# Optimization experiments

Measured on AMD Instinct MI355X. Metric: run time of the kernel, lower is better.

## Reference

```python
import jax, jax.numpy as jnp
import numpy as np


def _cdist(queries, data):
    # Euclidean distance matrix [m, n], matching torch.cdist(p=2)
    q2 = jnp.sum(queries * queries, axis=1)[:, None]
    d2 = jnp.sum(data * data, axis=1)[None, :]
    sq = q2 + d2 - 2.0 * (queries @ data.T)
    return jnp.sqrt(jnp.maximum(sq, 0.0))


def setup_inputs() -> dict:
    key = jax.random.key(0)
    k1, k2 = jax.random.split(key)
    data = jax.random.normal(k1, (16384, 3), dtype=jnp.float32)
    queries = jax.random.normal(k2, (16384, 3), dtype=jnp.float32)
    return {"data": data, "queries": queries, "n_neigbor": 32}


def reference(data, queries, n_neigbor):
    m = queries.shape[0]
    n = data.shape[0]
    dists = _cdist(queries, data)                      # [m, n]
    sorted_dist = jnp.sort(dists, axis=1)              # full row sort, as in original
    k = sorted_dist[:, n_neigbor]                      # (n_neigbor)-th smallest distance
    in_nbr = dists < k[:, None]                        # strictly-less -> exactly n_neigbor True per row (no ties)
    # nonzero() in the original emits column indices in ascending order per row.
    # Replicate with fixed shapes: map non-neighbors to sentinel n, sort, keep first n_neigbor.
    cols = jnp.where(in_nbr, jnp.arange(n, dtype=jnp.int64)[None, :], jnp.int64(n))
    neighbors_index = jnp.sort(cols, axis=1)[:, :n_neigbor].reshape(-1)  # [m * n_neigbor]
    counts = jnp.sum(in_nbr.astype(jnp.int64), axis=1)
    splits = jnp.concatenate([jnp.zeros((1,), dtype=jnp.int64), jnp.cumsum(counts)])  # [m+1]
    return neighbors_index, splits
```

## Files before the change

### kernel.cpp

```cpp
#include <hip/hip_runtime.h>
#include <stdint.h>

typedef unsigned long long u64;
typedef unsigned int u32;

#define NQ 16384
#define ND 16384
#define KNB 32
#define KK 33
#define SPLITS_BASE (NQ * KNB)
#define CAP 512
#define NRR (CAP / 64)
#define NWQ 4
#define G 36
#define G3 (G*G*G)
#define SCB ((G3 + 255) / 256)
#define FINF (__int_as_float(0x7f800000))


template<int BITS>
__device__ __forceinline__ int wave_sum_small(int v) {
    int tot = 0;
    #pragma unroll
    for (int b = 0; b < BITS; ++b)
        tot += (int)__popcll(__ballot((v >> b) & 1)) << b;
    return tot;
}
__device__ __forceinline__ float wave_max_f(float v) {
    #pragma unroll
    for (int s = 1; s < 64; s <<= 1) v = fmaxf(v, __shfl_xor(v, s, 64));
    return v;
}
__device__ __forceinline__ int wave_excl_prefix(int v, int lane) {
    int x = v;
    #pragma unroll
    for (int s = 1; s < 64; s <<= 1) {
        const int y = __shfl_up(x, s, 64);
        if (lane >= s) x += y;
    }
    return x - v;
}
__device__ __forceinline__ int iclamp(int v, int lo, int hi) {
    return v < lo ? lo : (v > hi ? hi : v);
}
__device__ __forceinline__ u32 fenc(float f) {
    const u32 u = __float_as_uint(f);
    return (u & 0x80000000u) ? ~u : (u | 0x80000000u);
}
__device__ __forceinline__ float fdec(u32 e) {
    const u32 u = (e & 0x80000000u) ? (e & 0x7fffffffu) : ~e;
    return __uint_as_float(u);
}

__device__ __forceinline__ float bisect_rank8(const float (&r)[NRR], int rank) {
    u32 lo = 0u, hi = 0x7f800000u;
    #pragma unroll 1
    while (lo < hi) {
        const u32 mid = (lo + hi) >> 1;
        const float pv = __uint_as_float(mid);
        int c = 0;
        #pragma unroll
        for (int j = 0; j < NRR; ++j) c += (r[j] <= pv) ? 1 : 0;
        const int tot = wave_sum_small<4>(c);
        if (tot >= rank) hi = mid; else lo = mid + 1;
    }
    return __uint_as_float(hi);
}

__device__ __forceinline__ void pool_prune(float* kp, u32* ip, int& cnt, float& Tk,
                                           int lane, u64 lt) {
    float m = FINF;
    #pragma unroll 1
    for (int j = lane; j < cnt; j += 64) m = fminf(m, kp[j]);
    const float M = wave_max_f(m);
    int nc = 0;
    #pragma unroll 1
    for (int j0 = 0; j0 < cnt; j0 += 64) {
        const int j = j0 + lane;
        const bool val = j < cnt;
        float k = FINF; u32 id = 0;
        if (val) { k = kp[j]; id = ip[j]; }
        const bool keep = val && (k <= M);
        const u64 mask = __ballot(keep);
        if (keep) {
            const int s = nc + (int)__popcll(mask & lt);
            kp[s] = k; ip[s] = id;
        }
        nc += (int)__popcll(mask);
    }
    cnt = nc; Tk = M;
}

__device__ __forceinline__ void pool_hard_prune(float* kp, u32* ip, int& cnt,
                                                int lane, u64 lt) {
    float r[NRR];
    #pragma unroll
    for (int j = 0; j < NRR; ++j) {
        const int s = j * 64 + lane;
        r[j] = (s < cnt) ? kp[s] : FINF;
    }
    const float v = bisect_rank8(r, 64);
    int nc = 0, eqs = 0;
    #pragma unroll 1
    for (int j0 = 0; j0 < cnt; j0 += 64) {
        const int j = j0 + lane;
        const bool val = j < cnt;
        float k = FINF; u32 id = 0;
        if (val) { k = kp[j]; id = ip[j]; }
        const bool lt_v = val && (k < v);
        const bool eq_v = val && (k == v);
        const u64 mlt = __ballot(lt_v);
        const u64 meq = __ballot(eq_v);
        const int poplt = (int)__popcll(mlt);
        const int popeq = (int)__popcll(meq);
        if (lt_v) { const int s = nc + (int)__popcll(mlt & lt); kp[s] = k; ip[s] = id; }
        if (eq_v) {
            const int pe = (int)__popcll(meq & lt);
            if (eqs + pe < 64) { const int s = nc + poplt + pe; kp[s] = k; ip[s] = id; }
        }
        int kept_eq = popeq;
        if (eqs + popeq > 64) kept_eq = (64 - eqs > 0) ? (64 - eqs) : 0;
        nc += poplt + kept_eq;
        eqs += popeq;
    }
    cnt = nc;
}

__global__ __launch_bounds__(256) void bbox_kernel(const float* __restrict__ data,
                                                   u32* __restrict__ bbe) {
    const int i = blockIdx.x * 256 + threadIdx.x;
    const int lane = threadIdx.x & 63;
    float x = data[3*i], y = data[3*i+1], z = data[3*i+2];
    float mnx = x, mny = y, mnz = z, mxx = x, mxy = y, mxz = z;
    #pragma unroll
    for (int s = 1; s < 64; s <<= 1) {
        mnx = fminf(mnx, __shfl_xor(mnx, s, 64)); mxx = fmaxf(mxx, __shfl_xor(mxx, s, 64));
        mny = fminf(mny, __shfl_xor(mny, s, 64)); mxy = fmaxf(mxy, __shfl_xor(mxy, s, 64));
        mnz = fminf(mnz, __shfl_xor(mnz, s, 64)); mxz = fmaxf(mxz, __shfl_xor(mxz, s, 64));
    }
    if (lane == 0) {
        atomicMin(&bbe[0], fenc(mnx)); atomicMin(&bbe[1], fenc(mny)); atomicMin(&bbe[2], fenc(mnz));
        atomicMax(&bbe[3], fenc(mxx)); atomicMax(&bbe[4], fenc(mxy)); atomicMax(&bbe[5], fenc(mxz));
    }
}

__device__ __forceinline__ void grid_geom(const u32* bbe, float& mnx, float& mny, float& mnz,
                                          float& hx, float& hy, float& hz) {
    mnx = fdec(bbe[0]); mny = fdec(bbe[1]); mnz = fdec(bbe[2]);
    hx = fmaxf((fdec(bbe[3]) - mnx) * (1.0f / G), 1e-20f);
    hy = fmaxf((fdec(bbe[4]) - mny) * (1.0f / G), 1e-20f);
    hz = fmaxf((fdec(bbe[5]) - mnz) * (1.0f / G), 1e-20f);
}

__device__ __forceinline__ u32 cell_of(const u32* bbe, float x, float y, float z) {
    float mnx, mny, mnz, hx, hy, hz;
    grid_geom(bbe, mnx, mny, mnz, hx, hy, hz);
    const int cx = iclamp((int)((x - mnx) / hx), 0, G-1);
    const int cy = iclamp((int)((y - mny) / hy), 0, G-1);
    const int cz = iclamp((int)((z - mnz) / hz), 0, G-1);
    return (u32)((cz * G + cy) * G + cx);
}

__global__ __launch_bounds__(256) void cellid_hist(const float* __restrict__ data,
                                                   const u32* __restrict__ bbe,
                                                   u32* __restrict__ hist) {
    const int i = blockIdx.x * 256 + threadIdx.x;
    atomicAdd(&hist[cell_of(bbe, data[3*i], data[3*i+1], data[3*i+2])], 1u);
}

__global__ __launch_bounds__(256) void scan_partial(const u32* __restrict__ hist,
                                                    u32* __restrict__ cstart,
                                                    u32* __restrict__ bsum) {
    __shared__ u32 lds[256];
    const int t = threadIdx.x;
    const int i = blockIdx.x * 256 + t;
    const u32 v = (i < G3) ? hist[i] : 0u;
    lds[t] = v;
    __syncthreads();
    u32 x = v;
    for (int off = 1; off < 256; off *= 2) {
        const u32 add = (t >= off) ? lds[t - off] : 0u;
        __syncthreads();
        x += add; lds[t] = x;
        __syncthreads();
    }
    if (i < G3) cstart[i] = x - v;
    if (t == 255) bsum[blockIdx.x] = x;
}

__global__ __launch_bounds__(256) void scan_bsums(u32* __restrict__ bsum) {
    __shared__ u32 lds[256];
    const int t = threadIdx.x;
    const u32 v = (t < SCB) ? bsum[t] : 0u;
    lds[t] = v;
    __syncthreads();
    u32 x = v;
    for (int off = 1; off < 256; off *= 2) {
        const u32 add = (t >= off) ? lds[t - off] : 0u;
        __syncthreads();
        x += add; lds[t] = x;
        __syncthreads();
    }
    if (t < SCB) bsum[t] = x - v;
}

__global__ __launch_bounds__(256) void scan_add(u32* __restrict__ cstart,
                                                u32* __restrict__ cursor,
                                                const u32* __restrict__ bsum) {
    const int i = blockIdx.x * 256 + threadIdx.x;
    if (i < G3) {
        const u32 val = cstart[i] + bsum[blockIdx.x];
        cstart[i] = val; cursor[i] = val;
    }
    if (i == 0) cstart[G3] = (u32)ND;
}

__global__ __launch_bounds__(256) void scatter(const float* __restrict__ data,
                                               const u32* __restrict__ bbe,
                                               u32* __restrict__ cursor,
                                               float4* __restrict__ pts) {
    const int i = blockIdx.x * 256 + threadIdx.x;
    const float x = data[3*i], y = data[3*i+1], z = data[3*i+2];
    const u32 pos = atomicAdd(&cursor[cell_of(bbe, x, y, z)], 1u);
    pts[pos] = make_float4(x, y, z, __uint_as_float((u32)i));
}

__global__ __launch_bounds__(256) void knn_grid(const float4* __restrict__ pts,
                                                const u32* __restrict__ cstart,
                                                const float* __restrict__ queries,
                                                const u32* __restrict__ bbe,
                                                int* __restrict__ out_nb,
                                                int* __restrict__ splits) {
    __shared__ float keyP[NWQ][CAP];
    __shared__ u32   idxP[NWQ][CAP];
    __shared__ int   accI[NWQ][KNB];

    const int lane = threadIdx.x & 63;
    const int wid  = threadIdx.x >> 6;
    const int q = blockIdx.x * NWQ + wid;
    const u64 lt = (1ull << lane) - 1ull;
    float* kp = keyP[wid];
    u32*   ip = idxP[wid];

    const float qx = queries[3*q], qy = queries[3*q+1], qz = queries[3*q+2];
    const float q2 = __fadd_rn(__fadd_rn(__fmul_rn(qx,qx), __fmul_rn(qy,qy)), __fmul_rn(qz,qz));

    float mnx, mny, mnz, hx, hy, hz;
    grid_geom(bbe, mnx, mny, mnz, hx, hy, hz);
    const float hmin = fminf(hx, fminf(hy, hz));
    const int cx = iclamp((int)((qx - mnx) / hx), 0, G-1);
    const int cy = iclamp((int)((qy - mny) / hy), 0, G-1);
    const int cz = iclamp((int)((qz - mnz) / hz), 0, G-1);

    float Tk = FINF;
    int cnt = 0;

    auto gather_batch = [&](int sA, int lA, int sB, int lB) {
        const int len = lA + lB;
        const int P = wave_excl_prefix(len, lane);
        const int T = __shfl(P + len, 63, 64);
        #pragma unroll 1
        for (int g0 = 0; g0 < T; g0 += 64) {
            const int pos = g0 + lane;
            const bool val = pos < T;
            int rsel = 0;
            #pragma unroll
            for (int st = 32; st >= 1; st >>= 1) {
                const int t = rsel + st;
                const int Pt = __shfl(P, t, 64);
                if (Pt <= pos) rsel = t;
            }
            const int Pr  = __shfl(P,  rsel, 64);
            const int sAr = __shfl(sA, rsel, 64);
            const int lAr = __shfl(lA, rsel, 64);
            const int sBr = __shfl(sB, rsel, 64);
            const int off = pos - Pr;
            const int pi = (off < lAr) ? (sAr + off) : (sBr + (off - lAr));
            float key = FINF; u32 oi = 0; bool acc = false;
            if (val) {
                const float4 w = pts[pi];
                oi = __float_as_uint(w.w);
                const float d2 = __fadd_rn(__fadd_rn(__fmul_rn(w.x,w.x), __fmul_rn(w.y,w.y)),
                                           __fmul_rn(w.z,w.z));
                const float dot = __fmaf_rn(qz, w.z, __fmaf_rn(qy, w.y, __fmul_rn(qx, w.x)));
                const float sq  = __fsub_rn(__fadd_rn(q2, d2), __fadd_rn(dot, dot));
                key = fmaxf(sq, 0.0f);
                acc = key <= Tk;
            }
            const u64 mask = __ballot(acc);
            if (mask) {
                if (acc) {
                    const int s = cnt + (int)__popcll(mask & lt);
                    kp[s] = key; ip[s] = oi;
                }
                cnt += (int)__popcll(mask);
                if (cnt > CAP - 64) {
                    pool_prune(kp, ip, cnt, Tk, lane, lt);
                    if (cnt > CAP - 64) pool_hard_prune(kp, ip, cnt, lane, lt);
                }
            }
        }
    };

    int W = 0;
    {
        int ccount = 0;
        while (ccount < KK && W < G) {
            ++W;
            const int side = 2*W + 1, nrows = side * side;
            ccount = 0;
            for (int r0 = 0; r0 < nrows; r0 += 64) {
                const int rid = r0 + lane;
                int len = 0;
                if (rid < nrows) {
                    const int dz = rid / side - W, dy = rid % side - W;
                    const int zz = cz + dz, yy = cy + dy;
                    if (zz >= 0 && zz < G && yy >= 0 && yy < G) {
                        const int xlo = cx - W < 0 ? 0 : cx - W;
                        const int xhi = cx + W > G-1 ? G-1 : cx + W;
                        const int rb = (zz * G + yy) * G;
                        len = (int)cstart[rb + xhi + 1] - (int)cstart[rb + xlo];
                    }
                }
                ccount += wave_sum_small<6>(len < 63 ? len : 63);
            }
        }
    }

    {
        const int side = 2*W + 1, nrows = side * side;
        for (int r0 = 0; r0 < nrows; r0 += 64) {
            const int rid = r0 + lane;
            int sA = 0, lA = 0;
            if (rid < nrows) {
                const int dz = rid / side - W, dy = rid % side - W;
                const int zz = cz + dz, yy = cy + dy;
                if (zz >= 0 && zz < G && yy >= 0 && yy < G) {
                    const int xlo = cx - W < 0 ? 0 : cx - W;
                    const int xhi = cx + W > G-1 ? G-1 : cx + W;
                    const int rb = (zz * G + yy) * G;
                    sA = (int)cstart[rb + xlo];
                    lA = (int)cstart[rb + xhi + 1] - sA;
                }
            }
            gather_batch(sA, lA, 0, 0);
        }
    }

    float k33b;
    if (cnt <= 64) {
        float v = (lane < cnt) ? kp[lane] : FINF;
        #pragma unroll
        for (int k = 2; k <= 64; k <<= 1) {
            #pragma unroll
            for (int j = k >> 1; j >= 1; j >>= 1) {
                const float o = __shfl_xor(v, j, 64);
                const bool up = ((lane & k) == 0);
                const bool keepmin = (((lane & j) == 0) == up);
                v = keepmin ? fminf(v, o) : fmaxf(v, o);
            }
        }
        k33b = __shfl(v, KK - 1, 64);
    } else {
        float r[NRR];
        #pragma unroll
        for (int j = 0; j < NRR; ++j) {
            const int s = j * 64 + lane;
            r[j] = (s < cnt) ? kp[s] : FINF;
        }
        k33b = bisect_rank8(r, KK);
    }

    {
        int nc = 0;
        #pragma unroll 1
        for (int j0 = 0; j0 < cnt; j0 += 64) {
            const int j = j0 + lane;
            const bool val = j < cnt;
            float k = FINF; u32 id = 0;
            if (val) { k = kp[j]; id = ip[j]; }
            const bool keep = val && (k <= k33b);
            const u64 mask = __ballot(keep);
            if (keep) {
                const int s = nc + (int)__popcll(mask & lt);
                kp[s] = k; ip[s] = id;
            }
            nc += (int)__popcll(mask);
        }
        cnt = nc; Tk = k33b;
    }

    const float R2m = __fmaf_rn(k33b, 1.0002f, 1e-3f);
    if (!(R2m < (float)W * (float)W * hmin * hmin)) {
        const float Rm = sqrtf(R2m);
        const int Dz = (int)fminf(floorf(Rm / hz) + 1.0f, (float)G);
        const int Dy = (int)fminf(floorf(Rm / hy) + 1.0f, (float)G);
        const int sidey = 2*Dy + 1;
        const int nrows = (2*Dz + 1) * sidey;
        for (int r0 = 0; r0 < nrows; r0 += 64) {
            const int rid = r0 + lane;
            int sA = 0, lA = 0, sB = 0, lB = 0;
            if (rid < nrows) {
                const int dz = rid / sidey - Dz;
                const int dy = rid % sidey - Dy;
                const int zz = cz + dz, yy = cy + dy;
                if (zz >= 0 && zz < G && yy >= 0 && yy < G) {
                    const int adz = dz < 0 ? -dz : dz;
                    const int ady = dy < 0 ? -dy : dy;
                    const float mz = (adz >= 1) ? (float)(adz - 1) * hz : 0.0f;
                    const float my = (ady >= 1) ? (float)(ady - 1) * hy : 0.0f;
                    const float rowmin2 = mz*mz + my*my;
                    if (rowmin2 <= R2m) {
                        const int dxr = (int)fminf(floorf(sqrtf(R2m - rowmin2) / hx) + 1.0f, (float)G);
                        const int xlo = cx - dxr < 0 ? 0 : cx - dxr;
                        const int xhi = cx + dxr > G-1 ? G-1 : cx + dxr;
                        if (xlo <= xhi) {
                            const int rb = (zz * G + yy) * G;
                            if (adz <= W && ady <= W) {
                                const int xhiA = (cx - W - 1 < xhi) ? cx - W - 1 : xhi;
                                const int xloB = (cx + W + 1 > xlo) ? cx + W + 1 : xlo;
                                if (xlo <= xhiA) {
                                    sA = (int)cstart[rb + xlo];
                                    lA = (int)cstart[rb + xhiA + 1] - sA;
                                }
                                if (xloB <= xhi) {
                                    sB = (int)cstart[rb + xloB];
                                    lB = (int)cstart[rb + xhi + 1] - sB;
                                }
                            } else {
                                sA = (int)cstart[rb + xlo];
                                lA = (int)cstart[rb + xhi + 1] - sA;
                            }
                        }
                    }
                }
            }
            gather_batch(sA, lA, sB, lB);
        }
    }

    float k33;
    if (cnt <= 64) {
        float v = (lane < cnt) ? kp[lane] : FINF;
        #pragma unroll
        for (int k = 2; k <= 64; k <<= 1) {
            #pragma unroll
            for (int j = k >> 1; j >= 1; j >>= 1) {
                const float o = __shfl_xor(v, j, 64);
                const bool up = ((lane & k) == 0);
                const bool keepmin = (((lane & j) == 0) == up);
                v = keepmin ? fminf(v, o) : fmaxf(v, o);
            }
        }
        k33 = __shfl(v, KK - 1, 64);
    } else {
        float r[NRR];
        #pragma unroll
        for (int j = 0; j < NRR; ++j) {
            const int s = j * 64 + lane;
            r[j] = (s < cnt) ? kp[s] : FINF;
        }
        k33 = bisect_rank8(r, KK);
    }

    const float kd = sqrtf(k33);
    float cut;
    if (!(kd > 0.0f)) {
        cut = -1.0f;
    } else {
        int bi = __float_as_int(__fmul_rn(kd, kd));
        #pragma unroll 1
        for (int s = 0; s < 8; ++s) {
            if (bi > 0 && sqrtf(__int_as_float(bi - 1)) >= kd) --bi; else break;
        }
        #pragma unroll 1
        for (int s = 0; s < 8; ++s) {
            if (sqrtf(__int_as_float(bi)) < kd) ++bi; else break;
        }
        cut = __int_as_float(bi);
    }

    int c = 0;
    #pragma unroll 1
    for (int j0 = 0; j0 < cnt; j0 += 64) {
        const int j = j0 + lane;
        const bool val = j < cnt;
        const float k = val ? kp[j] : FINF;
        const bool keep = val && (k < cut);
        const u64 mask = __ballot(keep);
        if (keep) {
            const int s = c + (int)__popcll(mask & lt);
            if (s < KNB) accI[wid][s] = (int)ip[j];
        }
        c += (int)__popcll(mask);
    }
    if (c > KNB) c = KNB;

    if (lane < KNB) {
        if (lane < c) {
            const int my = accI[wid][lane];
            int rank = 0;
            #pragma unroll 1
            for (int j = 0; j < KNB; ++j)
                if (j < c) rank += (accI[wid][j] < my) ? 1 : 0;
            out_nb[(size_t)q * KNB + rank] = my;
        } else {
            out_nb[(size_t)q * KNB + lane] = ND;
        }
    }
    if (lane == 0) splits[1 + q] = c;
}

__global__ __launch_bounds__(256) void knn_direct_kernel(const float* __restrict__ data,
                                                         const float* __restrict__ queries,
                                                         int* __restrict__ out_nb,
                                                         int* __restrict__ splits) {
    __shared__ float4 tile[1024];
    const int q = blockIdx.x * 256 + threadIdx.x;
    const float qx = queries[3*q], qy = queries[3*q+1], qz = queries[3*q+2];
    const float q2 = __fadd_rn(__fadd_rn(__fmul_rn(qx,qx), __fmul_rn(qy,qy)), __fmul_rn(qz,qz));
    float arrk[KK]; int arri[KK];
    for (int j = 0; j < KK; ++j) { arrk[j] = FINF; arri[j] = ND; }
    float cur_maxk = FINF;
    for (int t0 = 0; t0 < ND; t0 += 1024) {
        for (int p = threadIdx.x; p < 1024; p += 256) {
            const int g = t0 + p;
            const float x = data[3*g], y = data[3*g+1], z = data[3*g+2];
            const float d2 = __fadd_rn(__fadd_rn(__fmul_rn(x,x), __fmul_rn(y,y)), __fmul_rn(z,z));
            tile[p] = make_float4(x, y, z, d2);
        }
        __syncthreads();
        for (int p = 0; p < 1024; ++p) {
            const float4 dp = tile[p];
            const float dot = __fmaf_rn(qz, dp.z, __fmaf_rn(qy, dp.y, __fmul_rn(qx, dp.x)));
            const float sq  = __fsub_rn(__fadd_rn(q2, dp.w), __fadd_rn(dot, dot));
            const float key = fmaxf(sq, 0.0f);
            if (key < cur_maxk) {
                int mp = 0; float m = -1.0f;
                for (int j = 0; j < KK; ++j) if (arrk[j] > m) { m = arrk[j]; mp = j; }
                arrk[mp] = key; arri[mp] = t0 + p;
                m = -1.0f;
                for (int j = 0; j < KK; ++j) if (arrk[j] > m) m = arrk[j];
                cur_maxk = m;
            }
        }
        __syncthreads();
    }
    const float kdist = sqrtf(cur_maxk);
    int acc[KNB]; int c = 0;
    for (int j = 0; j < KK; ++j) {
        const float d = sqrtf(arrk[j]);
        if (d < kdist && c < KNB) acc[c++] = arri[j];
    }
    for (int a = 1; a < c; ++a) {
        const int v = acc[a]; int j = a;
        while (j > 0 && acc[j-1] > v) { acc[j] = acc[j-1]; --j; }
        acc[j] = v;
    }
    int* row = out_nb + (size_t)q * KNB;
    for (int j = 0; j < KNB; ++j) row[j] = (j < c) ? acc[j] : ND;
    splits[1 + q] = c;
}

__global__ __launch_bounds__(1024) void splits_scan_kernel(int* __restrict__ splits) {
    __shared__ int lds[1024];
    const int t = threadIdx.x;
    int v[16]; int s = 0;
    #pragma unroll
    for (int j = 0; j < 16; ++j) { v[j] = splits[1 + t*16 + j]; s += v[j]; }
    lds[t] = s;
    __syncthreads();
    for (int off = 1; off < 1024; off *= 2) {
        const int add = (t >= off) ? lds[t - off] : 0;
        __syncthreads();
        lds[t] += add;
        __syncthreads();
    }
    int run = lds[t] - s;
    #pragma unroll
    for (int j = 0; j < 16; ++j) { run += v[j]; splits[1 + t*16 + j] = run; }
    if (t == 0) splits[0] = 0;
}

extern "C" void kernel_launch(void* const* d_in, const int* in_sizes, int n_in,
                              void* d_out, int out_size, void* d_ws, size_t ws_size,
                              hipStream_t stream) {
    const float* data    = (const float*)d_in[0];
    const float* queries = (const float*)d_in[1];
    int* out    = (int*)d_out;
    int* splits = out + SPLITS_BASE;

    const size_t bb_off     = 0;
    const size_t hist_off   = 64;
    const size_t cstart_off = hist_off + (size_t)G3 * 4;
    const size_t cursor_off = cstart_off + (size_t)(G3 + 1) * 4;
    const size_t bsum_off   = cursor_off + (size_t)G3 * 4;
    size_t pts_off          = bsum_off + 256 * 4;
    pts_off = (pts_off + 255) & ~(size_t)255;
    const size_t need       = pts_off + (size_t)ND * 16;

    if (ws_size >= need) {
        u32*    bbe    = (u32*)((char*)d_ws + bb_off);
        u32*    hist   = (u32*)((char*)d_ws + hist_off);
        u32*    cstart = (u32*)((char*)d_ws + cstart_off);
        u32*    cursor = (u32*)((char*)d_ws + cursor_off);
        u32*    bsum   = (u32*)((char*)d_ws + bsum_off);
        float4* pts    = (float4*)((char*)d_ws + pts_off);

        hipMemsetAsync(bbe, 0xFF, 12, stream);
        hipMemsetAsync((char*)bbe + 12, 0x00, 12, stream);
        hipMemsetAsync(hist, 0x00, (size_t)G3 * 4, stream);
        hipLaunchKernelGGL(bbox_kernel, dim3(ND / 256), dim3(256), 0, stream, data, bbe);
        hipLaunchKernelGGL(cellid_hist, dim3(ND / 256), dim3(256), 0, stream, data, bbe, hist);
        hipLaunchKernelGGL(scan_partial, dim3(SCB), dim3(256), 0, stream, hist, cstart, bsum);
        hipLaunchKernelGGL(scan_bsums, dim3(1), dim3(256), 0, stream, bsum);
        hipLaunchKernelGGL(scan_add, dim3(SCB), dim3(256), 0, stream, cstart, cursor, bsum);
        hipLaunchKernelGGL(scatter, dim3(ND / 256), dim3(256), 0, stream, data, bbe, cursor, pts);
        hipLaunchKernelGGL(knn_grid, dim3(NQ / NWQ), dim3(256), 0, stream,
                           pts, cstart, queries, bbe, out, splits);
    } else {
        hipLaunchKernelGGL(knn_direct_kernel, dim3(NQ / 256), dim3(256), 0, stream,
                           data, queries, out, splits);
    }
    hipLaunchKernelGGL(splits_scan_kernel, dim3(1), dim3(1024), 0, stream, splits);
}
```

Measured before the change: 117.4 us.

## Fuse grid build into one cooperative kernel and halve waves per KNN block

Replaces the three memsets and six small build kernels (bbox, histogram, three scan stages, scatter) with one cooperative kernel that uses grid-wide syncs between phases. The aim is to remove the launch and inter-kernel gaps that dominate such tiny kernels. Separately, the KNN kernel now runs 2 waves per block instead of 4, giving smaller blocks and finer scheduling. Grid syncs carry their own cost, and cooperative launch needs all 256 blocks to be resident at once.

```diff
diff --git a/kernel.cpp b/kernel.cpp
--- a/kernel.cpp
+++ b/kernel.cpp
@@ -1,4 +1,5 @@
 #include <hip/hip_runtime.h>
+#include <hip/hip_cooperative_groups.h>
 #include <stdint.h>
 
 typedef unsigned long long u64;
@@ -11,10 +12,9 @@
 #define SPLITS_BASE (NQ * KNB)
 #define CAP 512
 #define NRR (CAP / 64)
-#define NWQ 4
+#define NWQ 2
 #define G 36
 #define G3 (G*G*G)
-#define SCB ((G3 + 255) / 256)
 #define FINF (__int_as_float(0x7f800000))
 
 
@@ -126,24 +126,6 @@
     cnt = nc;
 }
 
-__global__ __launch_bounds__(256) void bbox_kernel(const float* __restrict__ data,
-                                                   u32* __restrict__ bbe) {
-    const int i = blockIdx.x * 256 + threadIdx.x;
-    const int lane = threadIdx.x & 63;
-    float x = data[3*i], y = data[3*i+1], z = data[3*i+2];
-    float mnx = x, mny = y, mnz = z, mxx = x, mxy = y, mxz = z;
-    #pragma unroll
-    for (int s = 1; s < 64; s <<= 1) {
-        mnx = fminf(mnx, __shfl_xor(mnx, s, 64)); mxx = fmaxf(mxx, __shfl_xor(mxx, s, 64));
-        mny = fminf(mny, __shfl_xor(mny, s, 64)); mxy = fmaxf(mxy, __shfl_xor(mxy, s, 64));
-        mnz = fminf(mnz, __shfl_xor(mnz, s, 64)); mxz = fmaxf(mxz, __shfl_xor(mxz, s, 64));
-    }
-    if (lane == 0) {
-        atomicMin(&bbe[0], fenc(mnx)); atomicMin(&bbe[1], fenc(mny)); atomicMin(&bbe[2], fenc(mnz));
-        atomicMax(&bbe[3], fenc(mxx)); atomicMax(&bbe[4], fenc(mxy)); atomicMax(&bbe[5], fenc(mxz));
-    }
-}
-
 __device__ __forceinline__ void grid_geom(const u32* bbe, float& mnx, float& mny, float& mnz,
                                           float& hx, float& hy, float& hz) {
     mnx = fdec(bbe[0]); mny = fdec(bbe[1]); mnz = fdec(bbe[2]);
@@ -161,76 +143,95 @@
     return (u32)((cz * G + cy) * G + cx);
 }
 
-__global__ __launch_bounds__(256) void cellid_hist(const float* __restrict__ data,
-                                                   const u32* __restrict__ bbe,
-                                                   u32* __restrict__ hist) {
-    const int i = blockIdx.x * 256 + threadIdx.x;
-    atomicAdd(&hist[cell_of(bbe, data[3*i], data[3*i+1], data[3*i+2])], 1u);
-}
-
-__global__ __launch_bounds__(256) void scan_partial(const u32* __restrict__ hist,
-                                                    u32* __restrict__ cstart,
-                                                    u32* __restrict__ bsum) {
+__global__ __launch_bounds__(256) void build_all(const float* __restrict__ data,
+                                                 u32* __restrict__ bbe,
+                                                 u32* __restrict__ hist,
+                                                 u32* __restrict__ cstart,
+                                                 u32* __restrict__ cursor,
+                                                 u32* __restrict__ bsum,
+                                                 float4* __restrict__ pts) {
+    cooperative_groups::grid_group gg = cooperative_groups::this_grid();
     __shared__ u32 lds[256];
-    const int t = threadIdx.x;
-    const int i = blockIdx.x * 256 + t;
-    const u32 v = (i < G3) ? hist[i] : 0u;
-    lds[t] = v;
+    const int tid = threadIdx.x;
+    const int bid = blockIdx.x;
+    const int gt = bid * 256 + tid;
+    const int lane = tid & 63;
+
+    for (int i = gt; i < G3; i += 65536) hist[i] = 0u;
+    if (gt < 3) bbe[gt] = 0xFFFFFFFFu;
+    else if (gt < 6) bbe[gt] = 0u;
+    gg.sync();
+
+    if (gt < ND) {
+        float x = data[3*gt], y = data[3*gt+1], z = data[3*gt+2];
+        float mnx = x, mny = y, mnz = z, mxx = x, mxy = y, mxz = z;
+        #pragma unroll
+        for (int s = 1; s < 64; s <<= 1) {
+            mnx = fminf(mnx, __shfl_xor(mnx, s, 64)); mxx = fmaxf(mxx, __shfl_xor(mxx, s, 64));
+            mny = fminf(mny, __shfl_xor(mny, s, 64)); mxy = fmaxf(mxy, __shfl_xor(mxy, s, 64));
+            mnz = fminf(mnz, __shfl_xor(mnz, s, 64)); mxz = fmaxf(mxz, __shfl_xor(mxz, s, 64));
+        }
+        if (lane == 0) {
+            atomicMin(&bbe[0], fenc(mnx)); atomicMin(&bbe[1], fenc(mny)); atomicMin(&bbe[2], fenc(mnz));
+            atomicMax(&bbe[3], fenc(mxx)); atomicMax(&bbe[4], fenc(mxy)); atomicMax(&bbe[5], fenc(mxz));
+        }
+    }
+    gg.sync();
+
+    if (gt < ND)
+        atomicAdd(&hist[cell_of(bbe, data[3*gt], data[3*gt+1], data[3*gt+2])], 1u);
+    gg.sync();
+
+    const u32 hv = (gt < G3) ? hist[gt] : 0u;
+    lds[tid] = hv;
     __syncthreads();
-    u32 x = v;
+    u32 x = hv;
     for (int off = 1; off < 256; off *= 2) {
-        const u32 add = (t >= off) ? lds[t - off] : 0u;
-        __syncthreads();
-        x += add; lds[t] = x;
-        __syncthreads();
-    }
-    if (i < G3) cstart[i] = x - v;
-    if (t == 255) bsum[blockIdx.x] = x;
-}
-
-__global__ __launch_bounds__(256) void scan_bsums(u32* __restrict__ bsum) {
-    __shared__ u32 lds[256];
-    const int t = threadIdx.x;
-    const u32 v = (t < SCB) ? bsum[t] : 0u;
-    lds[t] = v;
-    __syncthreads();
-    u32 x = v;
-    for (int off = 1; off < 256; off *= 2) {
-        const u32 add = (t >= off) ? lds[t - off] : 0u;
-        __syncthreads();
-        x += add; lds[t] = x;
-        __syncthreads();
-    }
-    if (t < SCB) bsum[t] = x - v;
-}
-
-__global__ __launch_bounds__(256) void scan_add(u32* __restrict__ cstart,
-                                                u32* __restrict__ cursor,
-                                                const u32* __restrict__ bsum) {
-    const int i = blockIdx.x * 256 + threadIdx.x;
-    if (i < G3) {
-        const u32 val = cstart[i] + bsum[blockIdx.x];
-        cstart[i] = val; cursor[i] = val;
-    }
-    if (i == 0) cstart[G3] = (u32)ND;
-}
-
-__global__ __launch_bounds__(256) void scatter(const float* __restrict__ data,
-                                               const u32* __restrict__ bbe,
-                                               u32* __restrict__ cursor,
-                                               float4* __restrict__ pts) {
-    const int i = blockIdx.x * 256 + threadIdx.x;
-    const float x = data[3*i], y = data[3*i+1], z = data[3*i+2];
-    const u32 pos = atomicAdd(&cursor[cell_of(bbe, x, y, z)], 1u);
-    pts[pos] = make_float4(x, y, z, __uint_as_float((u32)i));
-}
-
-__global__ __launch_bounds__(256) void knn_grid(const float4* __restrict__ pts,
-                                                const u32* __restrict__ cstart,
-                                                const float* __restrict__ queries,
-                                                const u32* __restrict__ bbe,
-                                                int* __restrict__ out_nb,
-                                                int* __restrict__ splits) {
+        const u32 add = (tid >= off) ? lds[tid - off] : 0u;
+        __syncthreads();
+        x += add; lds[tid] = x;
+        __syncthreads();
+    }
+    if (gt < G3) cstart[gt] = x - hv;
+    if (tid == 255) bsum[bid] = x;
+    gg.sync();
+
+    {
+        const u32 bv = bsum[tid];
+        __syncthreads();
+        lds[tid] = bv;
+        __syncthreads();
+        u32 y = bv;
+        for (int off = 1; off < 256; off *= 2) {
+            const u32 add = (tid >= off) ? lds[tid - off] : 0u;
+            __syncthreads();
+            y += add; lds[tid] = y;
+            __syncthreads();
+        }
+        const u32 boff = lds[bid] - ((bid == tid) ? bv : 0u) - ((bid == tid) ? 0u : 0u);
+        const u32 excl = lds[bid] - bsum[bid];
+        if (gt < G3) {
+            const u32 val = (x - hv) + excl;
+            cstart[gt] = val; cursor[gt] = val;
+        }
+        if (gt == 0) cstart[G3] = (u32)ND;
+        (void)boff;
+    }
+    gg.sync();
+
+    if (gt < ND) {
+        const float px = data[3*gt], py = data[3*gt+1], pz = data[3*gt+2];
+        const u32 pos = atomicAdd(&cursor[cell_of(bbe, px, py, pz)], 1u);
+        pts[pos] = make_float4(px, py, pz, __uint_as_float((u32)gt));
+    }
+}
+
+__global__ __launch_bounds__(64 * NWQ) void knn_grid(const float4* __restrict__ pts,
+                                                     const u32* __restrict__ cstart,
+                                                     const float* __restrict__ queries,
+                                                     const u32* __restrict__ bbe,
+                                                     int* __restrict__ out_nb,
+                                                     int* __restrict__ splits) {
     __shared__ float keyP[NWQ][CAP];
     __shared__ u32   idxP[NWQ][CAP];
     __shared__ int   accI[NWQ][KNB];
@@ -607,16 +608,11 @@
         u32*    bsum   = (u32*)((char*)d_ws + bsum_off);
         float4* pts    = (float4*)((char*)d_ws + pts_off);
 
-        hipMemsetAsync(bbe, 0xFF, 12, stream);
-        hipMemsetAsync((char*)bbe + 12, 0x00, 12, stream);
-        hipMemsetAsync(hist, 0x00, (size_t)G3 * 4, stream);
-        hipLaunchKernelGGL(bbox_kernel, dim3(ND / 256), dim3(256), 0, stream, data, bbe);
-        hipLaunchKernelGGL(cellid_hist, dim3(ND / 256), dim3(256), 0, stream, data, bbe, hist);
-        hipLaunchKernelGGL(scan_partial, dim3(SCB), dim3(256), 0, stream, hist, cstart, bsum);
-        hipLaunchKernelGGL(scan_bsums, dim3(1), dim3(256), 0, stream, bsum);
-        hipLaunchKernelGGL(scan_add, dim3(SCB), dim3(256), 0, stream, cstart, cursor, bsum);
-        hipLaunchKernelGGL(scatter, dim3(ND / 256), dim3(256), 0, stream, data, bbe, cursor, pts);
-        hipLaunchKernelGGL(knn_grid, dim3(NQ / NWQ), dim3(256), 0, stream,
+        void* args[] = { (void*)&data, (void*)&bbe, (void*)&hist, (void*)&cstart,
+                         (void*)&cursor, (void*)&bsum, (void*)&pts };
+        hipLaunchCooperativeKernel((const void*)build_all, dim3(256), dim3(256),
+                                   args, 0, stream);
+        hipLaunchKernelGGL(knn_grid, dim3(NQ / NWQ), dim3(64 * NWQ), 0, stream,
                            pts, cstart, queries, bbe, out, splits);
     } else {
         hipLaunchKernelGGL(knn_direct_kernel, dim3(NQ / 256), dim3(256), 0, stream,
```

New measurement: 220.1 us. +87.4%, slower.

## Fold memsets and block-sum scan into neighbouring kernels, halve knn block size

Applied to the files above, without the earlier changes.

Encodes the bounding-box max as a negated min so a single 0xFF memset initialises all six entries. The histogram zeroing moves into bbox_kernel, and the block-sum scan is recomputed redundantly inside each scan_add block, which removes two memsets and one kernel launch. knn_grid now runs two query waves per block instead of four, giving smaller blocks and less LDS per block. The trade is redundant scan work in every scan_add block in return for fewer launches on a short pipeline.

```diff
diff --git a/kernel.cpp b/kernel.cpp
--- a/kernel.cpp
+++ b/kernel.cpp
@@ -11,7 +11,7 @@
 #define SPLITS_BASE (NQ * KNB)
 #define CAP 512
 #define NRR (CAP / 64)
-#define NWQ 4
+#define NWQ 2
 #define G 36
 #define G3 (G*G*G)
 #define SCB ((G3 + 255) / 256)
@@ -126,30 +126,13 @@
     cnt = nc;
 }
 
-__global__ __launch_bounds__(256) void bbox_kernel(const float* __restrict__ data,
-                                                   u32* __restrict__ bbe) {
-    const int i = blockIdx.x * 256 + threadIdx.x;
-    const int lane = threadIdx.x & 63;
-    float x = data[3*i], y = data[3*i+1], z = data[3*i+2];
-    float mnx = x, mny = y, mnz = z, mxx = x, mxy = y, mxz = z;
-    #pragma unroll
-    for (int s = 1; s < 64; s <<= 1) {
-        mnx = fminf(mnx, __shfl_xor(mnx, s, 64)); mxx = fmaxf(mxx, __shfl_xor(mxx, s, 64));
-        mny = fminf(mny, __shfl_xor(mny, s, 64)); mxy = fmaxf(mxy, __shfl_xor(mxy, s, 64));
-        mnz = fminf(mnz, __shfl_xor(mnz, s, 64)); mxz = fmaxf(mxz, __shfl_xor(mxz, s, 64));
-    }
-    if (lane == 0) {
-        atomicMin(&bbe[0], fenc(mnx)); atomicMin(&bbe[1], fenc(mny)); atomicMin(&bbe[2], fenc(mnz));
-        atomicMax(&bbe[3], fenc(mxx)); atomicMax(&bbe[4], fenc(mxy)); atomicMax(&bbe[5], fenc(mxz));
-    }
-}
-
 __device__ __forceinline__ void grid_geom(const u32* bbe, float& mnx, float& mny, float& mnz,
                                           float& hx, float& hy, float& hz) {
     mnx = fdec(bbe[0]); mny = fdec(bbe[1]); mnz = fdec(bbe[2]);
-    hx = fmaxf((fdec(bbe[3]) - mnx) * (1.0f / G), 1e-20f);
-    hy = fmaxf((fdec(bbe[4]) - mny) * (1.0f / G), 1e-20f);
-    hz = fmaxf((fdec(bbe[5]) - mnz) * (1.0f / G), 1e-20f);
+    const float mxx = -fdec(bbe[3]), mxy = -fdec(bbe[4]), mxz = -fdec(bbe[5]);
+    hx = fmaxf((mxx - mnx) * (1.0f / G), 1e-20f);
+    hy = fmaxf((mxy - mny) * (1.0f / G), 1e-20f);
+    hz = fmaxf((mxz - mnz) * (1.0f / G), 1e-20f);
 }
 
 __device__ __forceinline__ u32 cell_of(const u32* bbe, float x, float y, float z) {
@@ -159,6 +142,26 @@
     const int cy = iclamp((int)((y - mny) / hy), 0, G-1);
     const int cz = iclamp((int)((z - mnz) / hz), 0, G-1);
     return (u32)((cz * G + cy) * G + cx);
+}
+
+__global__ __launch_bounds__(256) void bbox_kernel(const float* __restrict__ data,
+                                                   u32* __restrict__ bbe,
+                                                   u32* __restrict__ hist) {
+    const int i = blockIdx.x * 256 + threadIdx.x;
+    for (int h = i; h < G3; h += ND) hist[h] = 0u;
+    const int lane = threadIdx.x & 63;
+    const float x = data[3*i], y = data[3*i+1], z = data[3*i+2];
+    float mnx = x, mny = y, mnz = z, nx = -x, ny = -y, nz = -z;
+    #pragma unroll
+    for (int s = 1; s < 64; s <<= 1) {
+        mnx = fminf(mnx, __shfl_xor(mnx, s, 64)); nx = fminf(nx, __shfl_xor(nx, s, 64));
+        mny = fminf(mny, __shfl_xor(mny, s, 64)); ny = fminf(ny, __shfl_xor(ny, s, 64));
+        mnz = fminf(mnz, __shfl_xor(mnz, s, 64)); nz = fminf(nz, __shfl_xor(nz, s, 64));
+    }
+    if (lane == 0) {
+        atomicMin(&bbe[0], fenc(mnx)); atomicMin(&bbe[1], fenc(mny)); atomicMin(&bbe[2], fenc(mnz));
+        atomicMin(&bbe[3], fenc(nx));  atomicMin(&bbe[4], fenc(ny));  atomicMin(&bbe[5], fenc(nz));
+    }
 }
 
 __global__ __launch_bounds__(256) void cellid_hist(const float* __restrict__ data,
@@ -188,28 +191,26 @@
     if (t == 255) bsum[blockIdx.x] = x;
 }
 
-__global__ __launch_bounds__(256) void scan_bsums(u32* __restrict__ bsum) {
-    __shared__ u32 lds[256];
-    const int t = threadIdx.x;
-    const u32 v = (t < SCB) ? bsum[t] : 0u;
-    lds[t] = v;
-    __syncthreads();
-    u32 x = v;
-    for (int off = 1; off < 256; off *= 2) {
-        const u32 add = (t >= off) ? lds[t - off] : 0u;
-        __syncthreads();
-        x += add; lds[t] = x;
-        __syncthreads();
-    }
-    if (t < SCB) bsum[t] = x - v;
-}
-
 __global__ __launch_bounds__(256) void scan_add(u32* __restrict__ cstart,
                                                 u32* __restrict__ cursor,
                                                 const u32* __restrict__ bsum) {
-    const int i = blockIdx.x * 256 + threadIdx.x;
+    __shared__ u32 lds[256];
+    const int t = threadIdx.x;
+    const u32 bv = (t < SCB) ? bsum[t] : 0u;
+    lds[t] = bv;
+    __syncthreads();
+    u32 y = bv;
+    for (int off = 1; off < 256; off *= 2) {
+        const u32 add = (t >= off) ? lds[t - off] : 0u;
+        __syncthreads();
+        y += add; lds[t] = y;
+        __syncthreads();
+    }
+    const u32 excl = lds[blockIdx.x] - ((blockIdx.x < SCB) ? bsum[blockIdx.x] : 0u);
+    __syncthreads();
+    const int i = blockIdx.x * 256 + t;
     if (i < G3) {
-        const u32 val = cstart[i] + bsum[blockIdx.x];
+        const u32 val = cstart[i] + excl;
         cstart[i] = val; cursor[i] = val;
     }
     if (i == 0) cstart[G3] = (u32)ND;
@@ -225,12 +226,12 @@
     pts[pos] = make_float4(x, y, z, __uint_as_float((u32)i));
 }
 
-__global__ __launch_bounds__(256) void knn_grid(const float4* __restrict__ pts,
-                                                const u32* __restrict__ cstart,
-                                                const float* __restrict__ queries,
-                                                const u32* __restrict__ bbe,
-                                                int* __restrict__ out_nb,
-                                                int* __restrict__ splits) {
+__global__ __launch_bounds__(64 * NWQ) void knn_grid(const float4* __restrict__ pts,
+                                                     const u32* __restrict__ cstart,
+                                                     const float* __restrict__ queries,
+                                                     const u32* __restrict__ bbe,
+                                                     int* __restrict__ out_nb,
+                                                     int* __restrict__ splits) {
     __shared__ float keyP[NWQ][CAP];
     __shared__ u32   idxP[NWQ][CAP];
     __shared__ int   accI[NWQ][KNB];
@@ -607,16 +608,13 @@
         u32*    bsum   = (u32*)((char*)d_ws + bsum_off);
         float4* pts    = (float4*)((char*)d_ws + pts_off);
 
-        hipMemsetAsync(bbe, 0xFF, 12, stream);
-        hipMemsetAsync((char*)bbe + 12, 0x00, 12, stream);
-        hipMemsetAsync(hist, 0x00, (size_t)G3 * 4, stream);
-        hipLaunchKernelGGL(bbox_kernel, dim3(ND / 256), dim3(256), 0, stream, data, bbe);
+        hipMemsetAsync(bbe, 0xFF, 24, stream);
+        hipLaunchKernelGGL(bbox_kernel, dim3(ND / 256), dim3(256), 0, stream, data, bbe, hist);
         hipLaunchKernelGGL(cellid_hist, dim3(ND / 256), dim3(256), 0, stream, data, bbe, hist);
         hipLaunchKernelGGL(scan_partial, dim3(SCB), dim3(256), 0, stream, hist, cstart, bsum);
-        hipLaunchKernelGGL(scan_bsums, dim3(1), dim3(256), 0, stream, bsum);
         hipLaunchKernelGGL(scan_add, dim3(SCB), dim3(256), 0, stream, cstart, cursor, bsum);
         hipLaunchKernelGGL(scatter, dim3(ND / 256), dim3(256), 0, stream, data, bbe, cursor, pts);
-        hipLaunchKernelGGL(knn_grid, dim3(NQ / NWQ), dim3(256), 0, stream,
+        hipLaunchKernelGGL(knn_grid, dim3(NQ / NWQ), dim3(64 * NWQ), 0, stream,
                            pts, cstart, queries, bbe, out, splits);
     } else {
         hipLaunchKernelGGL(knn_direct_kernel, dim3(NQ / 256), dim3(256), 0, stream,
```

After: 111.7 us. 4.9% less time.
